# Optimization experiments

Measured on AMD Instinct MI355X. Metric: run time of the kernel, lower is better.

The kernel has to match this reference:

```python
import jax, jax.numpy as jnp
import numpy as np

NB, NX, NU, NY, NQ = 16384, 512, 256, 128, 256


def setup_inputs() -> dict:
    key = jax.random.key(0)
    ks = jax.random.split(key, 13)
    s = 0.02  # small weight scale keeps the tanh recurrence well-behaved
    x = jax.random.normal(ks[0], (NB, NX), jnp.float32)
    u = jax.random.normal(ks[1], (NB, NU), jnp.float32)
    F = jax.random.normal(ks[2], (NX, NX), jnp.float32) * s
    B1 = jax.random.normal(ks[3], (NX, NQ), jnp.float32) * s
    B2 = jax.random.normal(ks[4], (NX, NU), jnp.float32) * s
    C1 = jax.random.normal(ks[5], (NQ, NX), jnp.float32) * s
    C2 = jax.random.normal(ks[6], (NY, NX), jnp.float32) * s
    D11 = jax.random.normal(ks[7], (NQ, NQ), jnp.float32) * s
    D12 = jax.random.normal(ks[8], (NQ, NU), jnp.float32) * s
    D21 = jax.random.normal(ks[9], (NY, NQ), jnp.float32) * s
    # E must be invertible (torch.inverse(self.E)); identity + small perturbation
    E = jnp.eye(NX, dtype=jnp.float32) + 0.05 * jax.random.normal(ks[10], (NX, NX), jnp.float32)
    # Lambda diagonal, positive (only Lambda[k,k] is used in _solve_w)
    lam = jax.random.uniform(ks[11], (NQ,), jnp.float32, minval=0.5, maxval=1.5)
    bv = jnp.zeros((NQ,), jnp.float32)  # bias=False -> bv is zeros
    return dict(x=x, u=u, F=F, B1=B1, B2=B2, C1=C1, C2=C2, D11=D11,
                D12=D12, D21=D21, E=E, lam=lam, bv=bv)


def _solve_w(x, u, C1, D11, D12, lam, bv):
    # Sequential forward-substitution over the nq nonlinear states:
    #   v_k = (x@C1[k] + w@D11[k] + u@D12[k] + bv[k]) / Lambda[k,k];  w_k = tanh(v_k)
    nb = x.shape[0]
    nq = lam.shape[0]
    # x/u contributions do not depend on w: precompute once. [nb, nq]
    xu = x @ C1.T + u @ D12.T + bv[None, :]

    def step(w, inp):
        d11_row, xu_k, lam_k, k = inp
        v_k = (xu_k + w @ d11_row) / lam_k          # [nb]
        w = w.at[:, k].set(jnp.tanh(v_k))
        return w, None

    w0 = jnp.zeros((nb, nq), x.dtype)
    w, _ = jax.lax.scan(step, w0, (D11, xu.T, lam, jnp.arange(nq)))
    return w


def reference(x, u, F, B1, B2, C1, C2, D11, D12, D21, E, lam, bv):
    w = _solve_w(x, u, C1, D11, D12, lam, bv)
    E_inv = jnp.linalg.inv(E)
    dx = x @ (E_inv @ F).T + w @ (E_inv @ B1).T + u @ (E_inv @ B2).T
    # linear_output path (no feedthrough: D22 term omitted as in default D22=0)
    y = x @ C2.T + w @ D21.T
    return dx, y
```

## Files before the change

### kernel.cpp

```cpp
#include <hip/hip_runtime.h>

#define NBq 16384
#define NXq 512
#define NUq 256
#define NYq 128
#define NQq 256
#define KP  1024
#define AUGW 1536

typedef __attribute__((ext_vector_type(8))) short short8;
typedef __attribute__((ext_vector_type(4))) float f32x4;

__device__ __forceinline__ ushort f2bf(float f) {
  uint x = __float_as_uint(f);
  x += 0x7FFFu + ((x >> 16) & 1u);
  return (ushort)(x >> 16);
}

#define GLOAD_LDS16(g, l)                                             \
  __builtin_amdgcn_global_load_lds(                                   \
      (const __attribute__((address_space(1))) void*)(g),             \
      (__attribute__((address_space(3))) void*)(l), 16, 0, 0)

__device__ __forceinline__ float rdlane(float x, int l) {
  return __int_as_float(__builtin_amdgcn_readlane(__float_as_int(x), l));
}

__global__ __launch_bounds__(256) void k_prep(const float* __restrict__ x, const float* __restrict__ u,
                                              const float* __restrict__ E, const float* __restrict__ F,
                                              const float* __restrict__ B1, const float* __restrict__ B2,
                                              const float* __restrict__ C1, const float* __restrict__ C2,
                                              const float* __restrict__ D11, const float* __restrict__ D12,
                                              const float* __restrict__ D21,
                                              ushort* __restrict__ P, float* __restrict__ AUG,
                                              ushort* __restrict__ Wxu, ushort* __restrict__ D11B,
                                              ushort* __restrict__ Wfull) {
  int b = blockIdx.x, tid = threadIdx.x;
  if (b < 12288) {
    int idx = b * 256 + tid;
    const int nx4 = NBq * NXq / 4;
    if (idx < nx4) {
      float4 v = *(const float4*)(x + (size_t)idx * 4);
      int row = idx >> 7, c4 = idx & 127;
      ushort4 h = { f2bf(v.x), f2bf(v.y), f2bf(v.z), f2bf(v.w) };
      *(ushort4*)(P + (size_t)row * KP + c4 * 4) = h;
    } else {
      int i = idx - nx4;
      float4 v = *(const float4*)(u + (size_t)i * 4);
      int row = i >> 6, c4 = i & 63;
      ushort4 h = { f2bf(v.x), f2bf(v.y), f2bf(v.z), f2bf(v.w) };
      *(ushort4*)(P + (size_t)row * KP + 768 + c4 * 4) = h;
    }
  } else if (b < 15360) {
    int idx = (b - 12288) * 256 + tid;
    int r = idx / AUGW, c = idx % AUGW;
    float v;
    if (c < 512)       v = E[r * 512 + c];
    else if (c < 1024) v = F[r * 512 + (c - 512)];
    else if (c < 1280) v = B1[r * 256 + (c - 1024)];
    else               v = B2[r * 256 + (c - 1280)];
    AUG[idx] = v;
  } else if (b < 16384) {
    int idx = (b - 15360) * 256 + tid;
    int r = idx >> 10, k = idx & 1023;
    float v;
    if (k < 512)      v = C1[r * 512 + k];
    else if (k < 768) v = 0.f;
    else              v = D12[r * 256 + (k - 768)];
    Wxu[idx] = f2bf(v);
  } else if (b < 16640) {
    int idx = (b - 16384) * 256 + tid;
    D11B[idx] = f2bf(D11[idx]);
  } else {
    int idx = (b - 16640) * 256 + tid;
    int j = idx >> 10, k = idx & 1023;
    float v;
    if (k < 512)      v = C2[j * 512 + k];
    else if (k < 768) v = D21[j * 256 + (k - 512)];
    else              v = 0.f;
    Wfull[(size_t)(512 + j) * KP + k] = f2bf(v);
  }
}

#define WSTRIDE 264
#define TANH_K 2.8853900817779268f

struct Pre {
  f32x4 xuv;
  short8 b[8];
  f32x4 rl2, bv2;
// ... 47 lines not shown
  constexpr int kt = t * 16;
  constexpr int cmax = (t + 1) >> 1;
  if constexpr (t < 15)
    tile_loads<t + 1>(xu, D11B, lam, bv, lane, r0w, nxt);
  const int q = lane & 3, r2 = lane >> 2;
  const int q4 = q * 4;
  const float (*dT)[16] = d11T[t];
  float4 dvb0 = *(const float4*)(&dT[0][q4]);
  float4 dvb1 = *(const float4*)(&dT[1][q4]);
  float4 dvb2 = *(const float4*)(&dT[2][q4]);
  float4 dvb3 = *(const float4*)(&dT[3][q4]);
  f32x4 accM = cur.xuv;
  #pragma unroll
  for (int c = 0; c < cmax; ++c)
    accM = __builtin_amdgcn_mfma_f32_16x16x32_bf16(cur.b[c], whiF[c], accM, 0, 0, 0);
  f32x4 acc;
  acc[0] = __int_as_float(__builtin_amdgcn_ds_bpermute(bp4, __float_as_int(accM[0])));
  acc[1] = __int_as_float(__builtin_amdgcn_ds_bpermute(bp4, __float_as_int(accM[1])));
  acc[2] = __int_as_float(__builtin_amdgcn_ds_bpermute(bp4, __float_as_int(accM[2])));
  acc[3] = __int_as_float(__builtin_amdgcn_ds_bpermute(bp4, __float_as_int(accM[3])));
  const f32x4 rl2 = cur.rl2, bv2 = cur.bv2;
  float wreg = 0.f, wk[4] = {0.f, 0.f, 0.f, 0.f};
  {
    float v_ = fmaf(acc[0], rl2[0], bv2[0]);
    float e_ = __builtin_amdgcn_exp2f(v_);
    float w_ = fmaf(-2.f, __builtin_amdgcn_rcpf(1.f + e_), 1.f);
    wreg = w_;
    if (q == 0) wk[0] = w_;
  }
  SOLVE_STEP(1, dvb0)
  SOLVE_STEP(2, dvb1)
  SOLVE_STEP(3, dvb2)
  SOLVE_STEP(4, dvb3)
  SOLVE_STEP(5, dvb0)
  SOLVE_STEP(6, dvb1)
  SOLVE_STEP(7, dvb2)
  SOLVE_STEP(8, dvb3)
  SOLVE_STEP(9, dvb0)
  SOLVE_STEP(10, dvb1)
  SOLVE_STEP(11, dvb2)
  SOLVE_STEP(12, dvb3)
  SOLVE_STEP(13, dvb0)
  SOLVE_STEP(14, dvb1)
  SOLVE_STEP(15, dvb2)
  ushort4 h = { f2bf(wk[0]), f2bf(wk[1]), f2bf(wk[2]), f2bf(wk[3]) };
  *(ushort4*)(wb + r2 * WSTRIDE + kt + q * 4) = h;
  if (((lane >> 4) >> 1) == (t & 1)) {
    constexpr int c = t >> 1;
    whiF[c] = *(const short8*)(wb + (lane & 15) * WSTRIDE + c * 32 + (lane >> 4) * 8);
  }
}

__global__ __launch_bounds__(256) void k_fused(const float* __restrict__ Ain, float* __restrict__ Aout,
                                               ushort* __restrict__ Wfull, int s, int ebase,
                                               ushort* __restrict__ P, const ushort* __restrict__ Wxu,
                                               float* __restrict__ xu,
                                               const float* __restrict__ D11,
                                               const ushort* __restrict__ D11B,
                                               const float* __restrict__ lam,
                                               const float* __restrict__ bv) {
  __shared__ __align__(16) char smem[69696];
  const int tid = threadIdx.x;
  const int wave = tid >> 6, lane = tid & 63;
  const int nby = 23 - s;
  const int last = (s == 7);

  if ((int)blockIdx.y < nby) {
    float (*M)[132] = (float (*)[132])smem;
    float (*sP)[68] = (float (*)[68])(smem + 33792);
    float (*sMC)[68] = (float (*)[68])(smem + 33792 + 17408);
    float (*pinv)[17] = (float (*)[17])(smem + 33792 + 2 * 17408);
    const int s64 = s * 64, r0 = blockIdx.x * 64, c0 = (s + 1 + blockIdx.y) * 64;
    const int r2 = tid >> 2, cq = (tid & 3) * 16;
    const int R4 = (tid >> 4) * 4;
    const int C4 = (tid & 15) * 4;
    const int C8 = (tid & 15) * 8;

    float av4[4][4];
    #pragma unroll
    for (int r = 0; r < 4; ++r) {
      float4 v = *(const float4*)(Ain + (size_t)(r0 + R4 + r) * AUGW + c0 + C4);
      av4[r][0] = v.x; av4[r][1] = v.y; av4[r][2] = v.z; av4[r][3] = v.w;
    }
    #pragma unroll
    for (int c4 = 0; c4 < 4; ++c4) {
      *(float4*)(&sP[r2][cq + c4 * 4]) =
          *(const float4*)(Ain + (size_t)(s64 + r2) * AUGW + c0 + cq + c4 * 4);
      *(float4*)(&sMC[r2][cq + c4 * 4]) =
          *(const float4*)(Ain + (size_t)(r0 + r2) * AUGW + s64 + cq + c4 * 4);
      *(float4*)(&M[r2][cq + c4 * 4]) =
          *(const float4*)(Ain + (size_t)(s64 + r2) * AUGW + s64 + cq + c4 * 4);
    }
    #pragma unroll
    for (int c = 0; c < 16; ++c)
      M[r2][64 + cq + c] = (r2 == cq + c) ? 1.f : 0.f;
    __syncthreads();

    for (int t = 0; t < 4; ++t) {
      const int kt = t * 16;
      if (wave == 0) {
        const int cc = lane & 31;
        float q[16];
        #pragma unroll
        for (int r = 0; r < 16; ++r)
          q[r] = (cc < 16) ? M[kt + r][kt + cc] : ((r == cc - 16) ? 1.f : 0.f);
        #pragma unroll
        for (int p = 0; p < 16; ++p) {
          float piv = rdlane(q[p], p);
          float rp = __builtin_amdgcn_rcpf(piv);
          rp = rp * (2.f - piv * rp);
          float a[16];
          #pragma unroll
          for (int r = 0; r < 16; ++r) a[r] = rdlane(q[r], p);
          q[p] *= rp;
          #pragma unroll
          for (int r = 0; r < 16; ++r)
            if (r != p) q[r] = fmaf(-a[r], q[p], q[r]);
        }
        if (lane >= 16 && lane < 32) {
          #pragma unroll
          for (int r = 0; r < 16; ++r) pinv[r][lane - 16] = q[r];
        }
      }
      __syncthreads();
      {
        const int ri = tid >> 4, j0 = (tid & 15) * 8;
        float rr[8] = {};
        float a0[8], a1[8], p0, p1;
        p0 = pinv[ri][0];
        #pragma unroll
        for (int c = 0; c < 8; c += 4)
          *(float4*)(&a0[c]) = *(const float4*)(&M[kt][j0 + c]);
        #pragma unroll
        for (int k = 0; k < 16; k += 2) {
          p1 = pinv[ri][k + 1];
          #pragma unroll
          for (int c = 0; c < 8; c += 4)
            *(float4*)(&a1[c]) = *(const float4*)(&M[kt + k + 1][j0 + c]);
          #pragma unroll
          for (int c = 0; c < 8; ++c) rr[c] = fmaf(p0, a0[c], rr[c]);
          if (k + 2 < 16) {
            p0 = pinv[ri][k + 2];
            #pragma unroll
            for (int c = 0; c < 8; c += 4)
              *(float4*)(&a0[c]) = *(const float4*)(&M[kt + k + 2][j0 + c]);
          }
          #pragma unroll
          for (int c = 0; c < 8; ++c) rr[c] = fmaf(p1, a1[c], rr[c]);
        }
        __syncthreads();
        #pragma unroll
        for (int c = 0; c < 8; c += 4)
          *(float4*)(&M[kt + ri][j0 + c]) = make_float4(rr[c], rr[c+1], rr[c+2], rr[c+3]);
      }
      __syncthreads();
      {
        const bool act = (wave != t);
        float mult[4][16], o2[4][8];
        if (act) {
          #pragma unroll
          for (int r = 0; r < 4; ++r) {
            #pragma unroll
            for (int j = 0; j < 4; ++j) {
              float4 m4 = *(const float4*)(&M[R4 + r][kt + 4 * j]);
              mult[r][4*j+0] = m4.x; mult[r][4*j+1] = m4.y;
              mult[r][4*j+2] = m4.z; mult[r][4*j+3] = m4.w;
            }
            float4 a = *(const float4*)(&M[R4 + r][C8]);
            float4 b = *(const float4*)(&M[R4 + r][C8 + 4]);
            o2[r][0] = a.x; o2[r][1] = a.y; o2[r][2] = a.z; o2[r][3] = a.w;
            o2[r][4] = b.x; o2[r][5] = b.y; o2[r][6] = b.z; o2[r][7] = b.w;
          }
        }
        __syncthreads();
        if (act) {
          float rv[2][8];
          {
            float4 a = *(const float4*)(&M[kt][C8]);
            float4 b = *(const float4*)(&M[kt][C8 + 4]);
            rv[0][0] = a.x; rv[0][1] = a.y; rv[0][2] = a.z; rv[0][3] = a.w;
            rv[0][4] = b.x; rv[0][5] = b.y; rv[0][6] = b.z; rv[0][7] = b.w;
          }
          #pragma unroll
          for (int k = 0; k < 16; ++k) {
            if (k + 1 < 16) {
              float4 a = *(const float4*)(&M[kt + k + 1][C8]);
              float4 b = *(const float4*)(&M[kt + k + 1][C8 + 4]);
              rv[(k+1)&1][0] = a.x; rv[(k+1)&1][1] = a.y;
              rv[(k+1)&1][2] = a.z; rv[(k+1)&1][3] = a.w;
              rv[(k+1)&1][4] = b.x; rv[(k+1)&1][5] = b.y;
              rv[(k+1)&1][6] = b.z; rv[(k+1)&1][7] = b.w;
            }
            #pragma unroll
            for (int r = 0; r < 4; ++r)
              #pragma unroll
              for (int c = 0; c < 8; ++c)
                o2[r][c] = fmaf(-mult[r][k], rv[k&1][c], o2[r][c]);
          }
          #pragma unroll
          for (int r = 0; r < 4; ++r) {
            *(float4*)(&M[R4 + r][C8]) =
                make_float4(o2[r][0], o2[r][1], o2[r][2], o2[r][3]);
            *(float4*)(&M[R4 + r][C8 + 4]) =
                make_float4(o2[r][4], o2[r][5], o2[r][6], o2[r][7]);
          }
        }
      }
      __syncthreads();
    }

    #define LOADCH_PB(dv, sv, ch)                                             \
      do {                                                                    \
        const int q0_ = (ch) * 4;                                             \
        _Pragma("unroll")                                                     \
        for (int r_ = 0; r_ < 4; ++r_) {                                      \
          float4 d_ = *(const float4*)(&M[R4 + r_][64 + q0_]);                \
          dv[r_][0] = d_.x; dv[r_][1] = d_.y; dv[r_][2] = d_.z; dv[r_][3] = d_.w; \
        }                                                                     \
        _Pragma("unroll")                                                     \
        for (int j_ = 0; j_ < 4; ++j_) {                                      \
          float4 s_ = *(const float4*)(&sP[q0_ + j_][C4]);                    \
          sv[j_][0] = s_.x; sv[j_][1] = s_.y; sv[j_][2] = s_.z; sv[j_][3] = s_.w; \
        }                                                                     \
      } while (0)
    #define LOADCH_MC(dv, sv, ch)                                             \
      do {                                                                    \
        const int q0_ = (ch) * 4;                                             \
        _Pragma("unroll")                                                     \
        for (int r_ = 0; r_ < 4; ++r_) {                                      \
          float4 d_ = *(const float4*)(&sMC[R4 + r_][q0_]);                   \
          dv[r_][0] = d_.x; dv[r_][1] = d_.y; dv[r_][2] = d_.z; dv[r_][3] = d_.w; \
        }                                                                     \
        _Pragma("unroll")                                                     \
        for (int j_ = 0; j_ < 4; ++j_) {                                      \
          float4 s_ = *(const float4*)(&sP[q0_ + j_][C4]);                    \
          sv[j_][0] = s_.x; sv[j_][1] = s_.y; sv[j_][2] = s_.z; sv[j_][3] = s_.w; \
        }                                                                     \
      } while (0)
    #define FMACH(acc, dv, sv, sgn)                                           \
      do {                                                                    \
        _Pragma("unroll")                                                     \
        for (int j_ = 0; j_ < 4; ++j_)                                        \
          _Pragma("unroll")                                                   \
          for (int r_ = 0; r_ < 4; ++r_)                                      \
            _Pragma("unroll")                                                 \
            for (int c_ = 0; c_ < 4; ++c_)                                    \
              acc[r_][c_] = fmaf(sgn dv[r_][j_], sv[j_][c_], acc[r_][c_]);    \
      } while (0)

    float pb[4][4] = {{0.f}};
    {
      float dvA[4][4], svA[4][4], dvB[4][4], svB[4][4];
      LOADCH_PB(dvA, svA, 0);
      #pragma unroll
      for (int ch = 0; ch < 16; ch += 2) {
        LOADCH_PB(dvB, svB, ch + 1);
        FMACH(pb, dvA, svA, +);
        if (ch + 2 < 16) LOADCH_PB(dvA, svA, ch + 2);
        FMACH(pb, dvB, svB, +);
      }
    }
    __syncthreads();
    #pragma unroll
    for (int r = 0; r < 4; ++r)
      *(float4*)(&sP[R4 + r][C4]) = make_float4(pb[r][0], pb[r][1], pb[r][2], pb[r][3]);
    __syncthreads();

    float o[4][4];
    if (blockIdx.x == (unsigned)s) {
      #pragma unroll
      for (int r = 0; r < 4; ++r)
        #pragma unroll
        for (int c = 0; c < 4; ++c) o[r][c] = pb[r][c];
    } else {
      #pragma unroll
      for (int r = 0; r < 4; ++r)
        #pragma unroll
        for (int c = 0; c < 4; ++c) o[r][c] = av4[r][c];
      float dvA[4][4], svA[4][4], dvB[4][4], svB[4][4];
      LOADCH_MC(dvA, svA, 0);
      #pragma unroll
      for (int ch = 0; ch < 16; ch += 2) {
        LOADCH_MC(dvB, svB, ch + 1);
        FMACH(o, dvA, svA, -);
        if (ch + 2 < 16) LOADCH_MC(dvA, svA, ch + 2);
        FMACH(o, dvB, svB, -);
      }
    }
    #undef LOADCH_PB
    #undef LOADCH_MC
    #undef FMACH
    if (last) {
      int k0 = c0 - 512 + C4;
      #pragma unroll
      for (int r = 0; r < 4; ++r) {
        ushort4 h = { f2bf(o[r][0]), f2bf(o[r][1]), f2bf(o[r][2]), f2bf(o[r][3]) };
        *(ushort4*)(Wfull + (size_t)(r0 + R4 + r) * KP + k0) = h;
      }
    } else {
      #pragma unroll
      for (int r = 0; r < 4; ++r)
        *(float4*)(Aout + (size_t)(r0 + R4 + r) * AUGW + c0 + C4) =
            make_float4(o[r][0], o[r][1], o[r][2], o[r][3]);
    }
    return;
  }

  const int g = ebase + ((int)blockIdx.y - nby) * 8 + (int)blockIdx.x;

  if (g < 256) {
    ushort* sA = (ushort*)smem;
    ushort* sB = (ushort*)(smem + 24576);
    const int mb = g >> 1, nb = g & 1;
    int wm = wave & 1, wn = wave >> 1;
    int m0 = mb * 128, n0 = nb * 128;
    int r16 = lane & 15, kq = lane >> 4;
    int lrow = lane >> 2, lseg = lane & 3;
    const ushort* gA0 = P + (size_t)(m0 + wave * 32 + lrow) * KP + lseg * 8;
    const ushort* gA1 = gA0 + 16 * KP;
    const ushort* gB0 = Wxu + (size_t)(n0 + wave * 32 + lrow) * KP + lseg * 8;
    const ushort* gB1 = gB0 + 16 * KP;

    #define STAGE_KB(bi, kb_)                                              \
      do {                                                                 \
        GLOAD_LDS16(gA0 + (kb_) * 32, sA + (bi) * 4096 + wave * 1024);     \
        GLOAD_LDS16(gA1 + (kb_) * 32, sA + (bi) * 4096 + wave * 1024 + 512); \
        GLOAD_LDS16(gB0 + (kb_) * 32, sB + (bi) * 4096 + wave * 1024);     \
        GLOAD_LDS16(gB1 + (kb_) * 32, sB + (bi) * 4096 + wave * 1024 + 512); \
      } while (0)

    f32x4 acc[4][4] = {};
    const int NKB = KP / 32;
    STAGE_KB(0, 0);
    STAGE_KB(1, 1);
    #pragma unroll
    for (int kb = 0; kb < NKB; ++kb) {
      const int bi = kb % 3;
      if (kb + 2 < NKB) {
        STAGE_KB((kb + 2) % 3, kb + 2);
        asm volatile("s_waitcnt vmcnt(8)" ::: "memory");
      } else if (kb + 2 == NKB) {
        asm volatile("s_waitcnt vmcnt(4)" ::: "memory");
      } else {
        asm volatile("s_waitcnt vmcnt(0)" ::: "memory");
      }
      __builtin_amdgcn_s_barrier();
      __builtin_amdgcn_sched_barrier(0);
      short8 af[4], bf[4];
      #pragma unroll
      for (int t = 0; t < 4; ++t) {
        af[t] = *(const short8*)(sA + bi * 4096 + (wm * 64 + t * 16 + r16) * 32 + kq * 8);
        bf[t] = *(const short8*)(sB + bi * 4096 + (wn * 64 + t * 16 + r16) * 32 + kq * 8);
      }
      #pragma unroll
      for (int mt = 0; mt < 4; ++mt)
        #pragma unroll
        for (int nt = 0; nt < 4; ++nt)
          acc[mt][nt] = __builtin_amdgcn_mfma_f32_16x16x32_bf16(af[mt], bf[nt], acc[mt][nt], 0, 0, 0);
      __builtin_amdgcn_sched_barrier(0);
      __builtin_amdgcn_s_barrier();
    }
    #undef STAGE_KB

    #pragma unroll
    for (int mt = 0; mt < 4; ++mt)
      #pragma unroll
      for (int nt = 0; nt < 4; ++nt)
        #pragma unroll
        for (int i = 0; i < 4; ++i) {
          int m = m0 + wm * 64 + mt * 16 + kq * 4 + i;
          int n = n0 + wn * 64 + nt * 16 + r16;
          xu[(size_t)m * NQq + n] = acc[mt][nt][i];
        }
    return;
  }

  if (g >= 336 && g < 592) {
    const int sid = g - 336;
    ushort* wB = (ushort*)smem;
    float (*d11T)[16][16] = (float (*)[16][16])(smem + 33792);
    const int r0w = sid * 64 + wave * 16;
    const int bp4 = (((lane >> 2) | ((lane & 3) << 4)) << 2);
    for (int i = tid; i < 4096; i += 256) {
      int tt = i >> 8, j = (i >> 4) & 15, c = i & 15;
      d11T[tt][j][c] = (c > j) ? D11[(size_t)(tt * 16 + c) * NQq + tt * 16 + j] : 0.f;
    }
    Pre pre0, pre1;
    tile_loads<0>(xu, D11B, lam, bv, lane, r0w, pre0);
    __syncthreads();
    ushort* wb = wB + wave * 16 * WSTRIDE;
    short8 whiF[8] = {};
    do_tile<0>(xu, D11B, lam, bv, wb, d11T, whiF, lane, bp4, r0w, pre0, pre1);
    do_tile<1>(xu, D11B, lam, bv, wb, d11T, whiF, lane, bp4, r0w, pre1, pre0);
    do_tile<2>(xu, D11B, lam, bv, wb, d11T, whiF, lane, bp4, r0w, pre0, pre1);
    do_tile<3>(xu, D11B, lam, bv, wb, d11T, whiF, lane, bp4, r0w, pre1, pre0);
    do_tile<4>(xu, D11B, lam, bv, wb, d11T, whiF, lane, bp4, r0w, pre0, pre1);
    do_tile<5>(xu, D11B, lam, bv, wb, d11T, whiF, lane, bp4, r0w, pre1, pre0);
    do_tile<6>(xu, D11B, lam, bv, wb, d11T, whiF, lane, bp4, r0w, pre0, pre1);
    do_tile<7>(xu, D11B, lam, bv, wb, d11T, whiF, lane, bp4, r0w, pre1, pre0);
    do_tile<8>(xu, D11B, lam, bv, wb, d11T, whiF, lane, bp4, r0w, pre0, pre1);
    do_tile<9>(xu, D11B, lam, bv, wb, d11T, whiF, lane, bp4, r0w, pre1, pre0);
    do_tile<10>(xu, D11B, lam, bv, wb, d11T, whiF, lane, bp4, r0w, pre0, pre1);
    do_tile<11>(xu, D11B, lam, bv, wb, d11T, whiF, lane, bp4, r0w, pre1, pre0);
    do_tile<12>(xu, D11B, lam, bv, wb, d11T, whiF, lane, bp4, r0w, pre0, pre1);
    do_tile<13>(xu, D11B, lam, bv, wb, d11T, whiF, lane, bp4, r0w, pre1, pre0);
    do_tile<14>(xu, D11B, lam, bv, wb, d11T, whiF, lane, bp4, r0w, pre0, pre1);
    do_tile<15>(xu, D11B, lam, bv, wb, d11T, whiF, lane, bp4, r0w, pre1, pre0);
    #pragma unroll
    for (int it = 0; it < 8; ++it) {
      int f = it * 64 + lane;
      int m = f >> 5, k8 = f & 31;
      uint4 v = *(const uint4*)(wb + m * WSTRIDE + k8 * 8);
      *(uint4*)(P + (size_t)(r0w + m) * KP + NXq + k8 * 8) = v;
    }
    return;
  }
}

__global__ __launch_bounds__(256) void k_gemm(const ushort* __restrict__ P, const ushort* __restrict__ W,
                                              float* __restrict__ out) {
  __shared__ ushort sA[3][128 * 32];
  __shared__ ushort sB[3][128 * 32];
  int tid = threadIdx.x;
  int lane = tid & 63, wave = tid >> 6;
  int wm = wave & 1, wn = wave >> 1;
  int m0 = blockIdx.x * 128;
  int n0 = blockIdx.y * 128;
  int r16 = lane & 15, kq = lane >> 4;
  int lrow = lane >> 2, lseg = lane & 3;
  const ushort* gA0 = P + (size_t)(m0 + wave * 32 + lrow) * KP + lseg * 8;
  const ushort* gA1 = gA0 + 16 * KP;
// ... 30 lines not shown
    for (int t = 0; t < 4; ++t) {
      af[t] = *(const short8*)(&sA[bi][(wm * 64 + t * 16 + r16) * 32 + kq * 8]);
      bf[t] = *(const short8*)(&sB[bi][(wn * 64 + t * 16 + r16) * 32 + kq * 8]);
    }
    #pragma unroll
    for (int mt = 0; mt < 4; ++mt)
      #pragma unroll
      for (int nt = 0; nt < 4; ++nt)
        acc[mt][nt] = __builtin_amdgcn_mfma_f32_16x16x32_bf16(af[mt], bf[nt], acc[mt][nt], 0, 0, 0);
    __builtin_amdgcn_sched_barrier(0);
    __builtin_amdgcn_s_barrier();
  }
  #undef STAGE_KB

  #pragma unroll
  for (int mt = 0; mt < 4; ++mt)
    #pragma unroll
    for (int nt = 0; nt < 4; ++nt)
      #pragma unroll
      for (int i = 0; i < 4; ++i) {
        int m = m0 + wm * 64 + mt * 16 + kq * 4 + i;
        int n = n0 + wn * 64 + nt * 16 + r16;
        float val = acc[mt][nt][i];
        if (n < NXq) out[(size_t)m * NXq + n] = val;
        else out[(size_t)NBq * NXq + (size_t)m * NYq + (n - NXq)] = val;
      }
}

extern "C" void kernel_launch(void* const* d_in, const int* in_sizes, int n_in,
                              void* d_out, int out_size, void* d_ws, size_t ws_size,
                              hipStream_t stream) {
  const float* x   = (const float*)d_in[0];
  const float* u   = (const float*)d_in[1];
  const float* F   = (const float*)d_in[2];
  const float* B1  = (const float*)d_in[3];
  const float* B2  = (const float*)d_in[4];
  const float* C1  = (const float*)d_in[5];
  const float* C2  = (const float*)d_in[6];
  const float* D11 = (const float*)d_in[7];
  const float* D12 = (const float*)d_in[8];
  const float* D21 = (const float*)d_in[9];
  const float* E   = (const float*)d_in[10];
  const float* lam = (const float*)d_in[11];
  const float* bv  = (const float*)d_in[12];

  char* ws = (char*)d_ws;
  ushort* P    = (ushort*)ws;
  float* xu    = (float*)(ws + (size_t)(32u << 20));
  float* AUG0  = (float*)(ws + (size_t)(48u << 20));
  float* AUG1  = (float*)(ws + (size_t)(52u << 20));
  ushort* Wfull = (ushort*)(ws + (size_t)(56u << 20));
  ushort* Wxu   = (ushort*)(ws + (size_t)(58u << 20));
  ushort* D11B  = (ushort*)(ws + (size_t)(59u << 20));
  float* out   = (float*)d_out;
  float* AUGbuf[2] = { AUG0, AUG1 };

  static const int ebase_tab[8] = {0, 72, 152, 240, 336, 440, 552, 672};

  k_prep<<<17152, 256, 0, stream>>>(x, u, E, F, B1, B2, C1, C2, D11, D12, D21,
                                    P, AUG0, Wxu, D11B, Wfull);
  for (int s = 0; s < 8; ++s)
    k_fused<<<dim3(8, 32), 256, 0, stream>>>(AUGbuf[s & 1], AUGbuf[(s + 1) & 1],
                                             Wfull, s, ebase_tab[s],
                                             P, Wxu, xu, D11, D11B, lam, bv);
  k_gemm<<<dim3(128, 5), 256, 0, stream>>>(P, Wfull, out);
}
```

Before: 325.4 us.

## Use 128-wide Gauss-Jordan panels to halve elimination launches for E inversion

Measured after the change: 460.9 us. +41.6%, slower.

```diff
diff --git a/kernel.cpp b/kernel.cpp
--- a/kernel.cpp
+++ b/kernel.cpp
@@ -189,51 +189,38 @@
 }
 
 __global__ __launch_bounds__(256) void k_fused(const float* __restrict__ Ain, float* __restrict__ Aout,
-                                               ushort* __restrict__ Wfull, int s, int ebase,
+                                               ushort* __restrict__ Wfull, int s, int npan, int ebase,
                                                ushort* __restrict__ P, const ushort* __restrict__ Wxu,
                                                float* __restrict__ xu,
                                                const float* __restrict__ D11,
                                                const ushort* __restrict__ D11B,
                                                const float* __restrict__ lam,
                                                const float* __restrict__ bv) {
-  __shared__ __align__(16) char smem[69696];
+  __shared__ __align__(16) char smem[152640];
   const int tid = threadIdx.x;
   const int wave = tid >> 6, lane = tid & 63;
-  const int nby = 23 - s;
-  const int last = (s == 7);
-
-  if ((int)blockIdx.y < nby) {
-    float (*M)[132] = (float (*)[132])smem;
-    float (*sP)[68] = (float (*)[68])(smem + 33792);
-    float (*sMC)[68] = (float (*)[68])(smem + 33792 + 17408);
-    float (*pinv)[17] = (float (*)[17])(smem + 33792 + 2 * 17408);
-    const int s64 = s * 64, r0 = blockIdx.x * 64, c0 = (s + 1 + blockIdx.y) * 64;
-    const int r2 = tid >> 2, cq = (tid & 3) * 16;
-    const int R4 = (tid >> 4) * 4;
-    const int C4 = (tid & 15) * 4;
-    const int C8 = (tid & 15) * 8;
-
-    float av4[4][4];
-    #pragma unroll
-    for (int r = 0; r < 4; ++r) {
-      float4 v = *(const float4*)(Ain + (size_t)(r0 + R4 + r) * AUGW + c0 + C4);
-      av4[r][0] = v.x; av4[r][1] = v.y; av4[r][2] = v.z; av4[r][3] = v.w;
-    }
-    #pragma unroll
-    for (int c4 = 0; c4 < 4; ++c4) {
-      *(float4*)(&sP[r2][cq + c4 * 4]) =
-          *(const float4*)(Ain + (size_t)(s64 + r2) * AUGW + c0 + cq + c4 * 4);
-      *(float4*)(&sMC[r2][cq + c4 * 4]) =
-          *(const float4*)(Ain + (size_t)(r0 + r2) * AUGW + s64 + cq + c4 * 4);
-      *(float4*)(&M[r2][cq + c4 * 4]) =
-          *(const float4*)(Ain + (size_t)(s64 + r2) * AUGW + s64 + cq + c4 * 4);
-    }
-    #pragma unroll
-    for (int c = 0; c < 16; ++c)
-      M[r2][64 + cq + c] = (r2 == cq + c) ? 1.f : 0.f;
+
+  if ((int)blockIdx.y < npan) {
+    float (*M)[260] = (float (*)[260])smem;
+    float (*sPc)[36] = (float (*)[36])(smem + 133120);
+    float (*pinv)[17] = (float (*)[17])(smem + 133120 + 18432);
+    const int s128 = s * 128, r0 = blockIdx.x * 128;
+    const int c0 = s128 + 128 + blockIdx.y * 64;
+
+    {
+      const int r = tid >> 1, h = (tid & 1) * 64;
+      const float* src = Ain + (size_t)(s128 + r) * AUGW + s128 + h;
+      #pragma unroll
+      for (int c = 0; c < 64; c += 4)
+        *(float4*)(&M[r][h + c]) = *(const float4*)(src + c);
+      #pragma unroll
+      for (int c = 0; c < 64; c += 4)
+        *(float4*)(&M[r][128 + h + c]) = make_float4(r == h + c, r == h + c + 1,
+                                                     r == h + c + 2, r == h + c + 3);
+    }
     __syncthreads();
 
-    for (int t = 0; t < 4; ++t) {
+    for (int t = 0; t < 8; ++t) {
       const int kt = t * 16;
       if (wave == 0) {
         const int cc = lane & 31;
@@ -261,189 +248,181 @@
       }
       __syncthreads();
       {
-        const int ri = tid >> 4, j0 = (tid & 15) * 8;
-        float rr[8] = {};
-        float a0[8], a1[8], p0, p1;
+        const int ri = tid >> 4, j0 = (tid & 15) * 16;
+        float rr[16] = {};
+        float a0[16], a1[16], p0, p1v;
         p0 = pinv[ri][0];
         #pragma unroll
-        for (int c = 0; c < 8; c += 4)
+        for (int c = 0; c < 16; c += 4)
           *(float4*)(&a0[c]) = *(const float4*)(&M[kt][j0 + c]);
         #pragma unroll
         for (int k = 0; k < 16; k += 2) {
-          p1 = pinv[ri][k + 1];
-          #pragma unroll
-          for (int c = 0; c < 8; c += 4)
+          p1v = pinv[ri][k + 1];
+          #pragma unroll
+          for (int c = 0; c < 16; c += 4)
             *(float4*)(&a1[c]) = *(const float4*)(&M[kt + k + 1][j0 + c]);
           #pragma unroll
-          for (int c = 0; c < 8; ++c) rr[c] = fmaf(p0, a0[c], rr[c]);
+          for (int c = 0; c < 16; ++c) rr[c] = fmaf(p0, a0[c], rr[c]);
           if (k + 2 < 16) {
             p0 = pinv[ri][k + 2];
             #pragma unroll
-            for (int c = 0; c < 8; c += 4)
+            for (int c = 0; c < 16; c += 4)
               *(float4*)(&a0[c]) = *(const float4*)(&M[kt + k + 2][j0 + c]);
           }
           #pragma unroll
-          for (int c = 0; c < 8; ++c) rr[c] = fmaf(p1, a1[c], rr[c]);
+          for (int c = 0; c < 16; ++c) rr[c] = fmaf(p1v, a1[c], rr[c]);
         }
         __syncthreads();
         #pragma unroll
-        for (int c = 0; c < 8; c += 4)
+        for (int c = 0; c < 16; c += 4)
           *(float4*)(&M[kt + ri][j0 + c]) = make_float4(rr[c], rr[c+1], rr[c+2], rr[c+3]);
       }
       __syncthreads();
       {
-        const bool act = (wave != t);
-        float mult[4][16], o2[4][8];
+        const int cl = 32 * (t >> 1);
+        const int rA = (tid & 63) * 2;
+        const int cb = cl + (tid >> 6) * 40;
+        const bool act = ((rA >> 4) != t);
+        float m0[16], m1[16], o0[40], o1[40];
         if (act) {
           #pragma unroll
-          for (int r = 0; r < 4; ++r) {
-            #pragma unroll
-            for (int j = 0; j < 4; ++j) {
-              float4 m4 = *(const float4*)(&M[R4 + r][kt + 4 * j]);
-              mult[r][4*j+0] = m4.x; mult[r][4*j+1] = m4.y;
-              mult[r][4*j+2] = m4.z; mult[r][4*j+3] = m4.w;
-            }
-            float4 a = *(const float4*)(&M[R4 + r][C8]);
-            float4 b = *(const float4*)(&M[R4 + r][C8 + 4]);
-            o2[r][0] = a.x; o2[r][1] = a.y; o2[r][2] = a.z; o2[r][3] = a.w;
-            o2[r][4] = b.x; o2[r][5] = b.y; o2[r][6] = b.z; o2[r][7] = b.w;
+          for (int j = 0; j < 16; j += 4) {
+            float4 v = *(const float4*)(&M[rA][kt + j]);
+            m0[j] = v.x; m0[j+1] = v.y; m0[j+2] = v.z; m0[j+3] = v.w;
+            float4 w = *(const float4*)(&M[rA + 1][kt + j]);
+            m1[j] = w.x; m1[j+1] = w.y; m1[j+2] = w.z; m1[j+3] = w.w;
+          }
+          #pragma unroll
+          for (int c = 0; c < 40; c += 4) {
+            float4 v = *(const float4*)(&M[rA][cb + c]);
+            o0[c] = v.x; o0[c+1] = v.y; o0[c+2] = v.z; o0[c+3] = v.w;
+            float4 w = *(const float4*)(&M[rA + 1][cb + c]);
+            o1[c] = w.x; o1[c+1] = w.y; o1[c+2] = w.z; o1[c+3] = w.w;
           }
         }
         __syncthreads();
         if (act) {
-          float rv[2][8];
-          {
-            float4 a = *(const float4*)(&M[kt][C8]);
-            float4 b = *(const float4*)(&M[kt][C8 + 4]);
-            rv[0][0] = a.x; rv[0][1] = a.y; rv[0][2] = a.z; rv[0][3] = a.w;
-            rv[0][4] = b.x; rv[0][5] = b.y; rv[0][6] = b.z; rv[0][7] = b.w;
+          #pragma unroll
+          for (int k = 0; k < 16; ++k) {
+            float rv[40];
+            #pragma unroll
+            for (int c = 0; c < 40; c += 4)
+              *(float4*)(&rv[c]) = *(const float4*)(&M[kt + k][cb + c]);
+            #pragma unroll
+            for (int c = 0; c < 40; ++c) {
+              o0[c] = fmaf(-m0[k], rv[c], o0[c]);
+              o1[c] = fmaf(-m1[k], rv[c], o1[c]);
+            }
           }
           #pragma unroll
-          for (int k = 0; k < 16; ++k) {
-            if (k + 1 < 16) {
-              float4 a = *(const float4*)(&M[kt + k + 1][C8]);
-              float4 b = *(const float4*)(&M[kt + k + 1][C8 + 4]);
-              rv[(k+1)&1][0] = a.x; rv[(k+1)&1][1] = a.y;
-              rv[(k+1)&1][2] = a.z; rv[(k+1)&1][3] = a.w;
-              rv[(k+1)&1][4] = b.x; rv[(k+1)&1][5] = b.y;
-              rv[(k+1)&1][6] = b.z; rv[(k+1)&1][7] = b.w;
-            }
+          for (int c = 0; c < 40; c += 4) {
+            *(float4*)(&M[rA][cb + c]) = make_float4(o0[c], o0[c+1], o0[c+2], o0[c+3]);
+            *(float4*)(&M[rA + 1][cb + c]) = make_float4(o1[c], o1[c+1], o1[c+2], o1[c+3]);
+          }
+        }
+      }
+      __syncthreads();
+    }
+
+    {
+      const int r = tid >> 1, h = (tid & 1) * 64;
+      const float* src = Ain + (size_t)(r0 + r) * AUGW + s128 + h;
+      #pragma unroll
+      for (int c = 0; c < 64; c += 4)
+        *(float4*)(&M[r][h + c]) = *(const float4*)(src + c);
+    }
+    __syncthreads();
+
+    const int R4b = (tid >> 3) * 4, C4b = (tid & 7) * 4;
+    #pragma unroll
+    for (int ch = 0; ch < 2; ++ch) {
+      const int cc0 = c0 + ch * 32;
+      {
+        const int k = tid >> 1, h16 = (tid & 1) * 16;
+        const float* src = Ain + (size_t)(s128 + k) * AUGW + cc0 + h16;
+        #pragma unroll
+        for (int c = 0; c < 16; c += 4)
+          *(float4*)(&sPc[k][h16 + c]) = *(const float4*)(src + c);
+      }
+      __syncthreads();
+      float pb[4][4] = {{0.f,0.f,0.f,0.f},{0.f,0.f,0.f,0.f},{0.f,0.f,0.f,0.f},{0.f,0.f,0.f,0.f}};
+      for (int k4 = 0; k4 < 128; k4 += 4) {
+        float dva[4][4], spa[4][4];
+        #pragma unroll
+        for (int r = 0; r < 4; ++r) {
+          float4 v = *(const float4*)(&M[R4b + r][128 + k4]);
+          dva[r][0] = v.x; dva[r][1] = v.y; dva[r][2] = v.z; dva[r][3] = v.w;
+        }
+        #pragma unroll
+        for (int kk = 0; kk < 4; ++kk) {
+          float4 v = *(const float4*)(&sPc[k4 + kk][C4b]);
+          spa[kk][0] = v.x; spa[kk][1] = v.y; spa[kk][2] = v.z; spa[kk][3] = v.w;
+        }
+        #pragma unroll
+        for (int kk = 0; kk < 4; ++kk)
+          #pragma unroll
+          for (int r = 0; r < 4; ++r)
+            #pragma unroll
+            for (int c = 0; c < 4; ++c)
+              pb[r][c] = fmaf(dva[r][kk], spa[kk][c], pb[r][c]);
+      }
+      __syncthreads();
+      #pragma unroll
+      for (int r = 0; r < 4; ++r)
+        *(float4*)(&sPc[R4b + r][C4b]) = make_float4(pb[r][0], pb[r][1], pb[r][2], pb[r][3]);
+      __syncthreads();
+      float o[4][4];
+      if (blockIdx.x == (unsigned)s) {
+        #pragma unroll
+        for (int r = 0; r < 4; ++r)
+          #pragma unroll
+          for (int c = 0; c < 4; ++c) o[r][c] = pb[r][c];
+      } else {
+        #pragma unroll
+        for (int r = 0; r < 4; ++r) {
+          float4 v = *(const float4*)(Ain + (size_t)(r0 + R4b + r) * AUGW + cc0 + C4b);
+          o[r][0] = v.x; o[r][1] = v.y; o[r][2] = v.z; o[r][3] = v.w;
+        }
+        for (int k4 = 0; k4 < 128; k4 += 4) {
+          float mca[4][4], spa[4][4];
+          #pragma unroll
+          for (int r = 0; r < 4; ++r) {
+            float4 v = *(const float4*)(&M[R4b + r][k4]);
+            mca[r][0] = v.x; mca[r][1] = v.y; mca[r][2] = v.z; mca[r][3] = v.w;
+          }
+          #pragma unroll
+          for (int kk = 0; kk < 4; ++kk) {
+            float4 v = *(const float4*)(&sPc[k4 + kk][C4b]);
+            spa[kk][0] = v.x; spa[kk][1] = v.y; spa[kk][2] = v.z; spa[kk][3] = v.w;
+          }
+          #pragma unroll
+          for (int kk = 0; kk < 4; ++kk)
             #pragma unroll
             for (int r = 0; r < 4; ++r)
               #pragma unroll
-              for (int c = 0; c < 8; ++c)
-                o2[r][c] = fmaf(-mult[r][k], rv[k&1][c], o2[r][c]);
-          }
-          #pragma unroll
-          for (int r = 0; r < 4; ++r) {
-            *(float4*)(&M[R4 + r][C8]) =
-                make_float4(o2[r][0], o2[r][1], o2[r][2], o2[r][3]);
-            *(float4*)(&M[R4 + r][C8 + 4]) =
-                make_float4(o2[r][4], o2[r][5], o2[r][6], o2[r][7]);
-          }
-        }
+              for (int c = 0; c < 4; ++c)
+                o[r][c] = fmaf(-mca[r][kk], spa[kk][c], o[r][c]);
+        }
+      }
+      if (s == 3) {
+        int k0 = cc0 - 512 + C4b;
+        #pragma unroll
+        for (int r = 0; r < 4; ++r) {
+          ushort4 h = { f2bf(o[r][0]), f2bf(o[r][1]), f2bf(o[r][2]), f2bf(o[r][3]) };
+          *(ushort4*)(Wfull + (size_t)(r0 + R4b + r) * KP + k0) = h;
+        }
+      } else {
+        #pragma unroll
+        for (int r = 0; r < 4; ++r)
+          *(float4*)(Aout + (size_t)(r0 + R4b + r) * AUGW + cc0 + C4b) =
+              make_float4(o[r][0], o[r][1], o[r][2], o[r][3]);
       }
       __syncthreads();
     }
-
-    #define LOADCH_PB(dv, sv, ch)                                             \
-      do {                                                                    \
-        const int q0_ = (ch) * 4;                                             \
-        _Pragma("unroll")                                                     \
-        for (int r_ = 0; r_ < 4; ++r_) {                                      \
-          float4 d_ = *(const float4*)(&M[R4 + r_][64 + q0_]);                \
-          dv[r_][0] = d_.x; dv[r_][1] = d_.y; dv[r_][2] = d_.z; dv[r_][3] = d_.w; \
-        }                                                                     \
-        _Pragma("unroll")                                                     \
-        for (int j_ = 0; j_ < 4; ++j_) {                                      \
-          float4 s_ = *(const float4*)(&sP[q0_ + j_][C4]);                    \
-          sv[j_][0] = s_.x; sv[j_][1] = s_.y; sv[j_][2] = s_.z; sv[j_][3] = s_.w; \
-        }                                                                     \
-      } while (0)
-    #define LOADCH_MC(dv, sv, ch)                                             \
-      do {                                                                    \
-        const int q0_ = (ch) * 4;                                             \
-        _Pragma("unroll")                                                     \
-        for (int r_ = 0; r_ < 4; ++r_) {                                      \
-          float4 d_ = *(const float4*)(&sMC[R4 + r_][q0_]);                   \
-          dv[r_][0] = d_.x; dv[r_][1] = d_.y; dv[r_][2] = d_.z; dv[r_][3] = d_.w; \
-        }                                                                     \
-        _Pragma("unroll")                                                     \
-        for (int j_ = 0; j_ < 4; ++j_) {                                      \
-          float4 s_ = *(const float4*)(&sP[q0_ + j_][C4]);                    \
-          sv[j_][0] = s_.x; sv[j_][1] = s_.y; sv[j_][2] = s_.z; sv[j_][3] = s_.w; \
-        }                                                                     \
-      } while (0)
-    #define FMACH(acc, dv, sv, sgn)                                           \
-      do {                                                                    \
-        _Pragma("unroll")                                                     \
-        for (int j_ = 0; j_ < 4; ++j_)                                        \
-          _Pragma("unroll")                                                   \
-          for (int r_ = 0; r_ < 4; ++r_)                                      \
-            _Pragma("unroll")                                                 \
-            for (int c_ = 0; c_ < 4; ++c_)                                    \
-              acc[r_][c_] = fmaf(sgn dv[r_][j_], sv[j_][c_], acc[r_][c_]);    \
-      } while (0)
-
-    float pb[4][4] = {{0.f}};
-    {
-      float dvA[4][4], svA[4][4], dvB[4][4], svB[4][4];
-      LOADCH_PB(dvA, svA, 0);
-      #pragma unroll
-      for (int ch = 0; ch < 16; ch += 2) {
-        LOADCH_PB(dvB, svB, ch + 1);
-        FMACH(pb, dvA, svA, +);
-        if (ch + 2 < 16) LOADCH_PB(dvA, svA, ch + 2);
-        FMACH(pb, dvB, svB, +);
-      }
-    }
-    __syncthreads();
-    #pragma unroll
-    for (int r = 0; r < 4; ++r)
-      *(float4*)(&sP[R4 + r][C4]) = make_float4(pb[r][0], pb[r][1], pb[r][2], pb[r][3]);
-    __syncthreads();
-
-    float o[4][4];
-    if (blockIdx.x == (unsigned)s) {
-      #pragma unroll
-      for (int r = 0; r < 4; ++r)
-        #pragma unroll
-        for (int c = 0; c < 4; ++c) o[r][c] = pb[r][c];
-    } else {
-      #pragma unroll
-      for (int r = 0; r < 4; ++r)
-        #pragma unroll
-        for (int c = 0; c < 4; ++c) o[r][c] = av4[r][c];
-      float dvA[4][4], svA[4][4], dvB[4][4], svB[4][4];
-      LOADCH_MC(dvA, svA, 0);
-      #pragma unroll
-      for (int ch = 0; ch < 16; ch += 2) {
-        LOADCH_MC(dvB, svB, ch + 1);
-        FMACH(o, dvA, svA, -);
-        if (ch + 2 < 16) LOADCH_MC(dvA, svA, ch + 2);
-        FMACH(o, dvB, svB, -);
-      }
-    }
-    #undef LOADCH_PB
-    #undef LOADCH_MC
-    #undef FMACH
-    if (last) {
-      int k0 = c0 - 512 + C4;
-      #pragma unroll
-      for (int r = 0; r < 4; ++r) {
-        ushort4 h = { f2bf(o[r][0]), f2bf(o[r][1]), f2bf(o[r][2]), f2bf(o[r][3]) };
-        *(ushort4*)(Wfull + (size_t)(r0 + R4 + r) * KP + k0) = h;
-      }
-    } else {
-      #pragma unroll
-      for (int r = 0; r < 4; ++r)
-        *(float4*)(Aout + (size_t)(r0 + R4 + r) * AUGW + c0 + C4) =
-            make_float4(o[r][0], o[r][1], o[r][2], o[r][3]);
-    }
     return;
   }
 
-  const int g = ebase + ((int)blockIdx.y - nby) * 8 + (int)blockIdx.x;
+  const int g = ebase + ((int)blockIdx.y - npan) * 4 + (int)blockIdx.x;
 
   if (g < 256) {
     ushort* sA = (ushort*)smem;
@@ -512,8 +491,8 @@
     return;
   }
 
-  if (g >= 336 && g < 592) {
-    const int sid = g - 336;
+  if (g >= 344 && g < 600) {
+    const int sid = g - 344;
     ushort* wB = (ushort*)smem;
     float (*d11T)[16][16] = (float (*)[16][16])(smem + 33792);
     const int r0w = sid * 64 + wave * 16;
@@ -653,13 +632,14 @@
   float* out   = (float*)d_out;
   float* AUGbuf[2] = { AUG0, AUG1 };
 
-  static const int ebase_tab[8] = {0, 72, 152, 240, 336, 440, 552, 672};
+  static const int npan_tab[4]  = {22, 20, 18, 16};
+  static const int ebase_tab[4] = {0, 168, 344, 528};
 
   k_prep<<<17152, 256, 0, stream>>>(x, u, E, F, B1, B2, C1, C2, D11, D12, D21,
                                     P, AUG0, Wxu, D11B, Wfull);
-  for (int s = 0; s < 8; ++s)
-    k_fused<<<dim3(8, 32), 256, 0, stream>>>(AUGbuf[s & 1], AUGbuf[(s + 1) & 1],
-                                             Wfull, s, ebase_tab[s],
+  for (int s = 0; s < 4; ++s)
+    k_fused<<<dim3(4, 64), 256, 0, stream>>>(AUGbuf[s & 1], AUGbuf[(s + 1) & 1],
+                                             Wfull, s, npan_tab[s], ebase_tab[s],
                                              P, Wxu, xu, D11, D11B, lam, bv);
   k_gemm<<<dim3(128, 5), 256, 0, stream>>>(P, Wfull, out);
 }
```

## Compute each stage's pivot-block inverse once and share it via global memory

Applied to the files above, without the earlier changes.

Result: slower. 342.4 us (+5.2%).

```diff
diff --git a/kernel.cpp b/kernel.cpp
--- a/kernel.cpp
+++ b/kernel.cpp
@@ -24,6 +24,124 @@
 
 __device__ __forceinline__ float rdlane(float x, int l) {
   return __int_as_float(__builtin_amdgcn_readlane(__float_as_int(x), l));
+}
+
+__device__ __forceinline__ void invert64(float (*M)[132], float (*pinv)[17], int tid) {
+  const int wave = tid >> 6, lane = tid & 63;
+  const int R4 = (tid >> 4) * 4;
+  const int C8 = (tid & 15) * 8;
+  for (int t = 0; t < 4; ++t) {
+    const int kt = t * 16;
+    if (wave == 0) {
+      const int cc = lane & 31;
+      float q[16];
+      #pragma unroll
+      for (int r = 0; r < 16; ++r)
+        q[r] = (cc < 16) ? M[kt + r][kt + cc] : ((r == cc - 16) ? 1.f : 0.f);
+      #pragma unroll
+      for (int p = 0; p < 16; ++p) {
+        float piv = rdlane(q[p], p);
+        float rp = __builtin_amdgcn_rcpf(piv);
+        rp = rp * (2.f - piv * rp);
+        float a[16];
+        #pragma unroll
+        for (int r = 0; r < 16; ++r) a[r] = rdlane(q[r], p);
+        q[p] *= rp;
+        #pragma unroll
+        for (int r = 0; r < 16; ++r)
+          if (r != p) q[r] = fmaf(-a[r], q[p], q[r]);
+      }
+      if (lane >= 16 && lane < 32) {
+        #pragma unroll
+        for (int r = 0; r < 16; ++r) pinv[r][lane - 16] = q[r];
+      }
+    }
+    __syncthreads();
+    {
+      const int ri = tid >> 4, j0 = (tid & 15) * 8;
+      float rr[8] = {};
+      float a0[8], a1[8], p0, p1;
+      p0 = pinv[ri][0];
+      #pragma unroll
+      for (int c = 0; c < 8; c += 4)
+        *(float4*)(&a0[c]) = *(const float4*)(&M[kt][j0 + c]);
+      #pragma unroll
+      for (int k = 0; k < 16; k += 2) {
+        p1 = pinv[ri][k + 1];
+        #pragma unroll
+        for (int c = 0; c < 8; c += 4)
+          *(float4*)(&a1[c]) = *(const float4*)(&M[kt + k + 1][j0 + c]);
+        #pragma unroll
+        for (int c = 0; c < 8; ++c) rr[c] = fmaf(p0, a0[c], rr[c]);
+        if (k + 2 < 16) {
+          p0 = pinv[ri][k + 2];
+          #pragma unroll
+          for (int c = 0; c < 8; c += 4)
+            *(float4*)(&a0[c]) = *(const float4*)(&M[kt + k + 2][j0 + c]);
+        }
+        #pragma unroll
+        for (int c = 0; c < 8; ++c) rr[c] = fmaf(p1, a1[c], rr[c]);
+      }
+      __syncthreads();
+      #pragma unroll
+      for (int c = 0; c < 8; c += 4)
+        *(float4*)(&M[kt + ri][j0 + c]) = make_float4(rr[c], rr[c+1], rr[c+2], rr[c+3]);
+    }
+    __syncthreads();
+    {
+      const bool act = (wave != t);
+      float mult[4][16], o2[4][8];
+      if (act) {
+        #pragma unroll
+        for (int r = 0; r < 4; ++r) {
+          #pragma unroll
+          for (int j = 0; j < 4; ++j) {
+            float4 m4 = *(const float4*)(&M[R4 + r][kt + 4 * j]);
+            mult[r][4*j+0] = m4.x; mult[r][4*j+1] = m4.y;
+            mult[r][4*j+2] = m4.z; mult[r][4*j+3] = m4.w;
+          }
+          float4 a = *(const float4*)(&M[R4 + r][C8]);
+          float4 b = *(const float4*)(&M[R4 + r][C8 + 4]);
+          o2[r][0] = a.x; o2[r][1] = a.y; o2[r][2] = a.z; o2[r][3] = a.w;
+          o2[r][4] = b.x; o2[r][5] = b.y; o2[r][6] = b.z; o2[r][7] = b.w;
+        }
+      }
+      __syncthreads();
+      if (act) {
+        float rv[2][8];
+        {
+          float4 a = *(const float4*)(&M[kt][C8]);
+          float4 b = *(const float4*)(&M[kt][C8 + 4]);
+          rv[0][0] = a.x; rv[0][1] = a.y; rv[0][2] = a.z; rv[0][3] = a.w;
+          rv[0][4] = b.x; rv[0][5] = b.y; rv[0][6] = b.z; rv[0][7] = b.w;
+        }
+        #pragma unroll
+        for (int k = 0; k < 16; ++k) {
+          if (k + 1 < 16) {
+            float4 a = *(const float4*)(&M[kt + k + 1][C8]);
+            float4 b = *(const float4*)(&M[kt + k + 1][C8 + 4]);
+            rv[(k+1)&1][0] = a.x; rv[(k+1)&1][1] = a.y;
+            rv[(k+1)&1][2] = a.z; rv[(k+1)&1][3] = a.w;
+            rv[(k+1)&1][4] = b.x; rv[(k+1)&1][5] = b.y;
+            rv[(k+1)&1][6] = b.z; rv[(k+1)&1][7] = b.w;
+          }
+          #pragma unroll
+          for (int r = 0; r < 4; ++r)
+            #pragma unroll
+            for (int c = 0; c < 8; ++c)
+              o2[r][c] = fmaf(-mult[r][k], rv[k&1][c], o2[r][c]);
+        }
+        #pragma unroll
+        for (int r = 0; r < 4; ++r) {
+          *(float4*)(&M[R4 + r][C8]) =
+              make_float4(o2[r][0], o2[r][1], o2[r][2], o2[r][3]);
+          *(float4*)(&M[R4 + r][C8 + 4]) =
+              make_float4(o2[r][4], o2[r][5], o2[r][6], o2[r][7]);
+        }
+      }
+    }
+    __syncthreads();
+  }
 }
 
 __global__ __launch_bounds__(256) void k_prep(const float* __restrict__ x, const float* __restrict__ u,
@@ -34,8 +152,25 @@
                                               const float* __restrict__ D21,
                                               ushort* __restrict__ P, float* __restrict__ AUG,
                                               ushort* __restrict__ Wxu, ushort* __restrict__ D11B,
-                                              ushort* __restrict__ Wfull) {
+                                              ushort* __restrict__ Wfull, float* __restrict__ DinvG) {
+  __shared__ float Mi[64][132];
+  __shared__ float pinv[16][17];
   int b = blockIdx.x, tid = threadIdx.x;
+  if (b == 17152) {
+    const int r = tid >> 2, cq = (tid & 3) * 16;
+    #pragma unroll
+    for (int c = 0; c < 16; c += 4)
+      *(float4*)(&Mi[r][cq + c]) = *(const float4*)(E + (size_t)r * 512 + cq + c);
+    #pragma unroll
+    for (int c = 0; c < 16; ++c)
+      Mi[r][64 + cq + c] = (r == cq + c) ? 1.f : 0.f;
+    __syncthreads();
+    invert64(Mi, pinv, tid);
+    #pragma unroll
+    for (int c = 0; c < 16; c += 4)
+      *(float4*)(DinvG + (size_t)r * 64 + cq + c) = *(float4*)(&Mi[r][64 + cq + c]);
+    return;
+  }
   if (b < 12288) {
     int idx = b * 256 + tid;
     const int nx4 = NBq * NXq / 4;
@@ -195,8 +330,9 @@
                                                const float* __restrict__ D11,
                                                const ushort* __restrict__ D11B,
                                                const float* __restrict__ lam,
-                                               const float* __restrict__ bv) {
-  __shared__ __align__(16) char smem[69696];
+                                               const float* __restrict__ bv,
+                                               float* __restrict__ DinvG) {
+  __shared__ __align__(16) char smem[52288];
   const int tid = threadIdx.x;
   const int wave = tid >> 6, lane = tid & 63;
   const int nby = 23 - s;
@@ -205,13 +341,11 @@
   if ((int)blockIdx.y < nby) {
     float (*M)[132] = (float (*)[132])smem;
     float (*sP)[68] = (float (*)[68])(smem + 33792);
-    float (*sMC)[68] = (float (*)[68])(smem + 33792 + 17408);
-    float (*pinv)[17] = (float (*)[17])(smem + 33792 + 2 * 17408);
+    float (*pinv)[17] = (float (*)[17])(smem + 33792 + 17408);
     const int s64 = s * 64, r0 = blockIdx.x * 64, c0 = (s + 1 + blockIdx.y) * 64;
     const int r2 = tid >> 2, cq = (tid & 3) * 16;
     const int R4 = (tid >> 4) * 4;
     const int C4 = (tid & 15) * 4;
-    const int C8 = (tid & 15) * 8;
 
     float av4[4][4];
     #pragma unroll
@@ -223,128 +357,12 @@
     for (int c4 = 0; c4 < 4; ++c4) {
       *(float4*)(&sP[r2][cq + c4 * 4]) =
           *(const float4*)(Ain + (size_t)(s64 + r2) * AUGW + c0 + cq + c4 * 4);
-      *(float4*)(&sMC[r2][cq + c4 * 4]) =
+      *(float4*)(&M[r2][cq + c4 * 4]) =
           *(const float4*)(Ain + (size_t)(r0 + r2) * AUGW + s64 + cq + c4 * 4);
-      *(float4*)(&M[r2][cq + c4 * 4]) =
-          *(const float4*)(Ain + (size_t)(s64 + r2) * AUGW + s64 + cq + c4 * 4);
-    }
-    #pragma unroll
-    for (int c = 0; c < 16; ++c)
-      M[r2][64 + cq + c] = (r2 == cq + c) ? 1.f : 0.f;
+      *(float4*)(&M[r2][64 + cq + c4 * 4]) =
+          *(const float4*)(DinvG + (size_t)s * 4096 + (size_t)r2 * 64 + cq + c4 * 4);
+    }
     __syncthreads();
-
-    for (int t = 0; t < 4; ++t) {
-      const int kt = t * 16;
-      if (wave == 0) {
-        const int cc = lane & 31;
-        float q[16];
-        #pragma unroll
-        for (int r = 0; r < 16; ++r)
-          q[r] = (cc < 16) ? M[kt + r][kt + cc] : ((r == cc - 16) ? 1.f : 0.f);
-        #pragma unroll
-        for (int p = 0; p < 16; ++p) {
-          float piv = rdlane(q[p], p);
-          float rp = __builtin_amdgcn_rcpf(piv);
-          rp = rp * (2.f - piv * rp);
-          float a[16];
-          #pragma unroll
-          for (int r = 0; r < 16; ++r) a[r] = rdlane(q[r], p);
-          q[p] *= rp;
-          #pragma unroll
-          for (int r = 0; r < 16; ++r)
-            if (r != p) q[r] = fmaf(-a[r], q[p], q[r]);
-        }
-        if (lane >= 16 && lane < 32) {
-          #pragma unroll
-          for (int r = 0; r < 16; ++r) pinv[r][lane - 16] = q[r];
-        }
-      }
-      __syncthreads();
-      {
-        const int ri = tid >> 4, j0 = (tid & 15) * 8;
-        float rr[8] = {};
-        float a0[8], a1[8], p0, p1;
-        p0 = pinv[ri][0];
-        #pragma unroll
-        for (int c = 0; c < 8; c += 4)
-          *(float4*)(&a0[c]) = *(const float4*)(&M[kt][j0 + c]);
-        #pragma unroll
-        for (int k = 0; k < 16; k += 2) {
-          p1 = pinv[ri][k + 1];
-          #pragma unroll
-          for (int c = 0; c < 8; c += 4)
-            *(float4*)(&a1[c]) = *(const float4*)(&M[kt + k + 1][j0 + c]);
-          #pragma unroll
-          for (int c = 0; c < 8; ++c) rr[c] = fmaf(p0, a0[c], rr[c]);
-          if (k + 2 < 16) {
-            p0 = pinv[ri][k + 2];
-            #pragma unroll
-            for (int c = 0; c < 8; c += 4)
-              *(float4*)(&a0[c]) = *(const float4*)(&M[kt + k + 2][j0 + c]);
-          }
-          #pragma unroll
-          for (int c = 0; c < 8; ++c) rr[c] = fmaf(p1, a1[c], rr[c]);
-        }
-        __syncthreads();
-        #pragma unroll
-        for (int c = 0; c < 8; c += 4)
-          *(float4*)(&M[kt + ri][j0 + c]) = make_float4(rr[c], rr[c+1], rr[c+2], rr[c+3]);
-      }
-      __syncthreads();
-      {
-        const bool act = (wave != t);
-        float mult[4][16], o2[4][8];
-        if (act) {
-          #pragma unroll
-          for (int r = 0; r < 4; ++r) {
-            #pragma unroll
-            for (int j = 0; j < 4; ++j) {
-              float4 m4 = *(const float4*)(&M[R4 + r][kt + 4 * j]);
-              mult[r][4*j+0] = m4.x; mult[r][4*j+1] = m4.y;
-              mult[r][4*j+2] = m4.z; mult[r][4*j+3] = m4.w;
-            }
-            float4 a = *(const float4*)(&M[R4 + r][C8]);
-            float4 b = *(const float4*)(&M[R4 + r][C8 + 4]);
-            o2[r][0] = a.x; o2[r][1] = a.y; o2[r][2] = a.z; o2[r][3] = a.w;
-            o2[r][4] = b.x; o2[r][5] = b.y; o2[r][6] = b.z; o2[r][7] = b.w;
-          }
-        }
-        __syncthreads();
-        if (act) {
-          float rv[2][8];
-          {
-            float4 a = *(const float4*)(&M[kt][C8]);
-            float4 b = *(const float4*)(&M[kt][C8 + 4]);
-            rv[0][0] = a.x; rv[0][1] = a.y; rv[0][2] = a.z; rv[0][3] = a.w;
-            rv[0][4] = b.x; rv[0][5] = b.y; rv[0][6] = b.z; rv[0][7] = b.w;
-          }
-          #pragma unroll
-          for (int k = 0; k < 16; ++k) {
-            if (k + 1 < 16) {
-              float4 a = *(const float4*)(&M[kt + k + 1][C8]);
-              float4 b = *(const float4*)(&M[kt + k + 1][C8 + 4]);
-              rv[(k+1)&1][0] = a.x; rv[(k+1)&1][1] = a.y;
-              rv[(k+1)&1][2] = a.z; rv[(k+1)&1][3] = a.w;
-              rv[(k+1)&1][4] = b.x; rv[(k+1)&1][5] = b.y;
-              rv[(k+1)&1][6] = b.z; rv[(k+1)&1][7] = b.w;
-            }
-            #pragma unroll
-            for (int r = 0; r < 4; ++r)
-              #pragma unroll
-              for (int c = 0; c < 8; ++c)
-                o2[r][c] = fmaf(-mult[r][k], rv[k&1][c], o2[r][c]);
-          }
-          #pragma unroll
-          for (int r = 0; r < 4; ++r) {
-            *(float4*)(&M[R4 + r][C8]) =
-                make_float4(o2[r][0], o2[r][1], o2[r][2], o2[r][3]);
-            *(float4*)(&M[R4 + r][C8 + 4]) =
-                make_float4(o2[r][4], o2[r][5], o2[r][6], o2[r][7]);
-          }
-        }
-      }
-      __syncthreads();
-    }
 
     #define LOADCH_PB(dv, sv, ch)                                             \
       do {                                                                    \
@@ -365,7 +383,7 @@
         const int q0_ = (ch) * 4;                                             \
         _Pragma("unroll")                                                     \
         for (int r_ = 0; r_ < 4; ++r_) {                                      \
-          float4 d_ = *(const float4*)(&sMC[R4 + r_][q0_]);                   \
+          float4 d_ = *(const float4*)(&M[R4 + r_][q0_]);                     \
           dv[r_][0] = d_.x; dv[r_][1] = d_.y; dv[r_][2] = d_.z; dv[r_][3] = d_.w; \
         }                                                                     \
         _Pragma("unroll")                                                     \
@@ -439,6 +457,22 @@
       for (int r = 0; r < 4; ++r)
         *(float4*)(Aout + (size_t)(r0 + R4 + r) * AUGW + c0 + C4) =
             make_float4(o[r][0], o[r][1], o[r][2], o[r][3]);
+    }
+
+    if (s < 7 && blockIdx.x == (unsigned)(s + 1) && blockIdx.y == 0) {
+      __syncthreads();
+      #pragma unroll
+      for (int r = 0; r < 4; ++r)
+        *(float4*)(&M[R4 + r][C4]) = make_float4(o[r][0], o[r][1], o[r][2], o[r][3]);
+      #pragma unroll
+      for (int c = 0; c < 16; ++c)
+        M[r2][64 + cq + c] = (r2 == cq + c) ? 1.f : 0.f;
+      __syncthreads();
+      invert64(M, pinv, tid);
+      #pragma unroll
+      for (int c = 0; c < 16; c += 4)
+        *(float4*)(DinvG + (size_t)(s + 1) * 4096 + (size_t)r2 * 64 + cq + c) =
+            *(float4*)(&M[r2][64 + cq + c]);
     }
     return;
   }
@@ -650,16 +684,17 @@
   ushort* Wfull = (ushort*)(ws + (size_t)(56u << 20));
   ushort* Wxu   = (ushort*)(ws + (size_t)(58u << 20));
   ushort* D11B  = (ushort*)(ws + (size_t)(59u << 20));
+  float* DinvG  = (float*)(ws + (size_t)(60u << 20));
   float* out   = (float*)d_out;
   float* AUGbuf[2] = { AUG0, AUG1 };
 
   static const int ebase_tab[8] = {0, 72, 152, 240, 336, 440, 552, 672};
 
-  k_prep<<<17152, 256, 0, stream>>>(x, u, E, F, B1, B2, C1, C2, D11, D12, D21,
-                                    P, AUG0, Wxu, D11B, Wfull);
+  k_prep<<<17153, 256, 0, stream>>>(x, u, E, F, B1, B2, C1, C2, D11, D12, D21,
+                                    P, AUG0, Wxu, D11B, Wfull, DinvG);
   for (int s = 0; s < 8; ++s)
     k_fused<<<dim3(8, 32), 256, 0, stream>>>(AUGbuf[s & 1], AUGbuf[(s + 1) & 1],
                                              Wfull, s, ebase_tab[s],
-                                             P, Wxu, xu, D11, D11B, lam, bv);
+                                             P, Wxu, xu, D11, D11B, lam, bv, DinvG);
   k_gemm<<<dim3(128, 5), 256, 0, stream>>>(P, Wfull, out);
 }
```
